# Optimization experiments

Hardware: AMD Instinct MI355X
Metric: run time of the kernel (lower is better)

Reference implementation:

```python
import jax, jax.numpy as jnp
import numpy as np

B, H, W, C = 32, 128, 128, 128
WS, SS, NH = 2, 1, 8          # window_size, shift_size, num_heads
SZ = WS * WS                   # tokens per window (4)
HD = C // NH                   # head dim
NW = (H // WS) * (W // WS)     # windows per image


def _rel_pos_index():
    coords = np.stack(np.meshgrid(np.arange(WS), np.arange(WS), indexing='ij')).reshape(2, -1)
    rel = (coords[:, :, None] - coords[:, None, :]).transpose(1, 2, 0)
    rel[:, :, 0] += WS - 1
    rel[:, :, 1] += WS - 1
    rel[:, :, 0] *= 2 * WS - 1
    return rel.sum(-1).reshape(-1)  # [SZ*SZ]


def _attn_mask():
    # shifted-window mask, computed once on host (static constant)
    img = np.zeros((H, W))
    cnt = 0
    sl = (slice(0, -WS), slice(-WS, -SS), slice(-SS, None))
    for hs in sl:
        for ws_ in sl:
            img[hs, ws_] = cnt
            cnt += 1
    mw = img.reshape(H // WS, WS, W // WS, WS).transpose(0, 2, 1, 3).reshape(-1, SZ)  # [NW, SZ]
    diff = mw[:, None, :] - mw[:, :, None]
    return np.where(diff != 0, -100.0, 0.0).astype(np.float32)  # [NW, SZ, SZ]

_RPI = _rel_pos_index()
_MASK = _attn_mask()


def setup_inputs() -> dict:
    key = jax.random.key(0)
    ks = jax.random.split(key, 6)
    return {
        'x': jax.random.normal(ks[0], (B, H * W, C), jnp.float32),
        'qkv_w': jax.random.normal(ks[1], (C, 3 * C), jnp.float32) * 0.02,
        'qkv_b': jnp.zeros((3 * C,), jnp.float32),
        'proj_w': jax.random.normal(ks[2], (C, C), jnp.float32) * 0.02,
        'proj_b': jnp.zeros((C,), jnp.float32),
        'rpb_table': jax.random.normal(ks[3], (9, NH), jnp.float32) * 0.02,
        'gamma1': jnp.ones((C,), jnp.float32),
        'beta1': jnp.zeros((C,), jnp.float32),
        'gamma2': jnp.ones((C,), jnp.float32),
        'beta2': jnp.zeros((C,), jnp.float32),
        'mlp_w1': jax.random.normal(ks[4], (C, 256), jnp.float32) * 0.02,
        'mlp_b1': jnp.zeros((256,), jnp.float32),
        'mlp_w2': jax.random.normal(ks[5], (256, C), jnp.float32) * 0.02,
        'mlp_b2': jnp.zeros((C,), jnp.float32),
    }


def _ln(z, g, b):
    m = z.mean(-1, keepdims=True)
    v = ((z - m) ** 2).mean(-1, keepdims=True)
    return (z - m) * jax.lax.rsqrt(v + 1e-5) * g + b


def reference(x, qkv_w, qkv_b, proj_w, proj_b, rpb_table,
              gamma1, beta1, gamma2, beta2, mlp_w1, mlp_b1, mlp_w2, mlp_b2):
    mask = jnp.asarray(_MASK)                      # [NW, SZ, SZ]
    skip = x
    h = _ln(x, gamma1, beta1).reshape(B, H, W, C)
    h = jnp.roll(h, (-SS, -SS), axis=(1, 2))       # cyclic shift
    # window partition -> [B*NW, SZ, C]
    hw = h.reshape(B, H // WS, WS, W // WS, WS, C).transpose(0, 1, 3, 2, 4, 5).reshape(B * NW, SZ, C)
    qkv = (hw @ qkv_w + qkv_b).reshape(B * NW, SZ, 3, NH, HD).transpose(2, 0, 3, 1, 4)
    q, k, v = qkv[0] * (HD ** -0.5), qkv[1], qkv[2]
    attn = jnp.einsum('nhid,nhjd->nhij', q, k)     # [B*NW, NH, SZ, SZ]
    rpb = rpb_table[_RPI].reshape(SZ, SZ, NH).transpose(2, 0, 1)
    attn = attn + rpb[None]
    attn = attn.reshape(B, NW, NH, SZ, SZ) + mask[None, :, None]
    attn = jax.nn.softmax(attn, axis=-1).reshape(B * NW, NH, SZ, SZ)
    o = jnp.einsum('nhij,nhjd->nhid', attn, v).transpose(0, 2, 1, 3).reshape(B * NW, SZ, C)
    o = o @ proj_w + proj_b
    # window reverse -> [B, H, W, C]
    o = o.reshape(B, H // WS, W // WS, WS, WS, C).transpose(0, 1, 3, 2, 4, 5).reshape(B, H, W, C)
    o = jnp.roll(o, (SS, SS), axis=(1, 2)).reshape(B, H * W, C)
    h = skip + o
    skip2 = h
    m = _ln(h, gamma2, beta2)
    m = jax.nn.gelu(m @ mlp_w1 + mlp_b1, approximate=False) @ mlp_w2 + mlp_b2
    return skip2 + m
```

## Files before the change

kernel.cpp:

```cpp
#include <hip/hip_runtime.h>
#include <math.h>


typedef __attribute__((ext_vector_type(8))) short short8;
typedef __attribute__((ext_vector_type(8))) unsigned short ushort8;
typedef __attribute__((ext_vector_type(4))) unsigned short ushort4v;
typedef __attribute__((ext_vector_type(4))) float f32x4;

#define MFMA __builtin_amdgcn_mfma_f32_16x16x32_bf16

__device__ inline unsigned short f2bf(float f) {
  union { float f; unsigned u; } v; v.f = f;
  unsigned r = (v.u + 0x7fffu + ((v.u >> 16) & 1u)) >> 16;
  return (unsigned short)r;
}
__device__ inline float bf2f(unsigned short s) {
  union { unsigned u; float f; } v; v.u = ((unsigned)s) << 16;
  return v.f;
}
__device__ inline void ld16(const unsigned short* p, float* o) {
  ushort8 a = *(const ushort8*)p;
  ushort8 b = *(const ushort8*)(p + 8);
  #pragma unroll
  for (int t = 0; t < 8; ++t) { o[t] = bf2f(a[t]); o[8 + t] = bf2f(b[t]); }
}

namespace {

__global__ __launch_bounds__(256) void prep_weights(
    const float* __restrict__ qkv_w, const float* __restrict__ proj_w,
    const float* __restrict__ w1, const float* __restrict__ w2,
    unsigned short* __restrict__ ws)
{
  const int idx = blockIdx.x * 256 + threadIdx.x;
  float v;
  if (idx < 49152) {
    const int n = idx >> 7, k = idx & 127; v = qkv_w[k * 384 + n];
  } else if (idx < 65536) {
    const int l = idx - 49152; const int n = l >> 7, k = l & 127;
    v = proj_w[k * 128 + n];
  } else if (idx < 98304) {
    const int l = idx - 65536; const int n = l >> 7, k = l & 127;
    v = w1[k * 256 + n];
  } else {
    const int l = idx - 98304; const int n = l >> 8, k = l & 255;
    v = w2[k * 128 + n];
  }
  ws[idx] = f2bf(v);
}

__global__ __launch_bounds__(256, 3) void swin_fused(
    const float* __restrict__ x,
    const unsigned short* __restrict__ wsw,
    const float* __restrict__ qkv_b,
    const float* __restrict__ proj_b,
    const float* __restrict__ rpb,
    const float* __restrict__ g1,
    const float* __restrict__ b1,
    const float* __restrict__ g2,
    const float* __restrict__ bt2,
    const float* __restrict__ bias1,
    const float* __restrict__ bias2,
    float* __restrict__ out)
{
  __shared__ __align__(16) unsigned char smem[52480];
  int* gsrc = (int*)smem;
  unsigned short (*Asm)[136]  = (unsigned short(*)[136])(smem + 256);
  unsigned short (*qkvh)[200] = (unsigned short(*)[200])(smem + 17664);
  unsigned short (*ohsc)[72]  = (unsigned short(*)[72])(smem + 43264);
  unsigned short (*ys)[136]   = (unsigned short(*)[136])(smem + 256);
  unsigned short (*hid0)[72]  = (unsigned short(*)[72])(smem + 17664);
  unsigned short (*hid1)[72]  = (unsigned short(*)[72])(smem + 26880);

  const int tid = threadIdx.x;
  const int n0 = blockIdx.x * 16;

  {
    const int r = tid >> 2;
    const int part = tid & 3;
    const int n = n0 + (r >> 2);
    const int s = r & 3;
    const int b = n >> 12;
    const int rem = n & 4095;
    const int wh = rem >> 6, wwi = rem & 63;
    const int hp = (2 * wh + (s >> 1) + 1) & 127;
    const int wp = (2 * wwi + (s & 1) + 1) & 127;
    const int src = (b << 14) + (hp << 7) + wp;
    if (part == 0) gsrc[r] = src;
    const float4* xr = (const float4*)(x + (size_t)src * 128 + part * 32);
    float4 v[8];
    float sum = 0.f, ssq = 0.f;
    #pragma unroll
    for (int i = 0; i < 8; ++i) {
      v[i] = xr[i];
      sum += v[i].x + v[i].y + v[i].z + v[i].w;
      ssq += v[i].x * v[i].x + v[i].y * v[i].y + v[i].z * v[i].z + v[i].w * v[i].w;
    }
    sum += __shfl_xor(sum, 1, 4); sum += __shfl_xor(sum, 2, 4);
    ssq += __shfl_xor(ssq, 1, 4); ssq += __shfl_xor(ssq, 2, 4);
    const float mean = sum * 0.0078125f;
    const float var = ssq * 0.0078125f - mean * mean;
    const float rstd = rsqrtf(var + 1e-5f);
    const int c0 = part * 32;
    #pragma unroll
    for (int i = 0; i < 8; ++i) {
      const int c = c0 + i * 4;
      const float4 gv = *(const float4*)(g1 + c);
      const float4 bv = *(const float4*)(b1 + c);
      ushort4v h4;
      h4.x = f2bf((v[i].x - mean) * rstd * gv.x + bv.x);
      h4.y = f2bf((v[i].y - mean) * rstd * gv.y + bv.y);
      h4.z = f2bf((v[i].z - mean) * rstd * gv.z + bv.z);
      h4.w = f2bf((v[i].w - mean) * rstd * gv.w + bv.w);
      *(ushort4v*)&Asm[r][c] = h4;
    }
  }
  __syncthreads();

  const int lane = tid & 63;
  const int wave = tid >> 6;
  const int l15 = lane & 15;
  const int quad = lane >> 4;

  const unsigned short* qkv_wt = wsw;
  const unsigned short* proj_wt = wsw + 49152;

  f32x4 accp[4][2] = {};

  for (int g = 0; g < 2; ++g) {
    {
      f32x4 acc[4][3] = {};
      const int nq = g * 64 + wave * 16 + l15;
      const unsigned short* bq = qkv_wt + (size_t)nq * 128;
      const unsigned short* bk = qkv_wt + (size_t)(128 + nq) * 128;
      const unsigned short* bv = qkv_wt + (size_t)(256 + nq) * 128;
      #pragma unroll
      for (int ks = 0; ks < 4; ++ks) {
        const int k0 = ks * 32 + quad * 8;
        const short8 fq = *(const short8*)(bq + k0);
        const short8 fk = *(const short8*)(bk + k0);
        const short8 fv = *(const short8*)(bv + k0);
        #pragma unroll
        for (int rf = 0; rf < 4; ++rf) {
          const short8 af = *(const short8*)&Asm[rf * 16 + l15][k0];
          acc[rf][0] = MFMA(af, fq, acc[rf][0], 0, 0, 0);
          acc[rf][1] = MFMA(af, fk, acc[rf][1], 0, 0, 0);
          acc[rf][2] = MFMA(af, fv, acc[rf][2], 0, 0, 0);
        }
      }
      const float bbq = qkv_b[nq];
      const float bbk = qkv_b[128 + nq];
      const float bbv = qkv_b[256 + nq];
      #pragma unroll
      for (int rf = 0; rf < 4; ++rf) {
        #pragma unroll
        for (int r = 0; r < 4; ++r) {
          const int row = rf * 16 + quad * 4 + r;
          qkvh[row][wave * 16 + l15]       = f2bf((acc[rf][0][r] + bbq) * 0.25f);
          qkvh[row][64 + wave * 16 + l15]  = f2bf(acc[rf][1][r] + bbk);
          qkvh[row][128 + wave * 16 + l15] = f2bf(acc[rf][2][r] + bbv);
        }
      }
    }
    __syncthreads();

    {
      const int w = tid >> 4;
      const int hl = (tid >> 2) & 3;
      const int i = tid & 3;
      const int h = g * 4 + hl;
      const int row_i = 4 * w + i;
      const int n = n0 + w;
      const int rem = n & 4095;
      const int wh = rem >> 6, wwi = rem & 63;
      const int yi = 2 * wh + (i >> 1);
      const int xi = 2 * wwi + (i & 1);
      const int regi = ((yi < 126) ? 0 : ((yi == 126) ? 1 : 2)) * 3
                     + ((xi < 126) ? 0 : ((xi == 126) ? 1 : 2));
      float q[16];
      ld16(&qkvh[row_i][hl * 16], q);
      float p[4];
      #pragma unroll
      for (int j = 0; j < 4; ++j) {
        float kk[16];
        ld16(&qkvh[4 * w + j][64 + hl * 16], kk);
        float d = 0.f;
        #pragma unroll
        for (int dd = 0; dd < 16; ++dd) d += q[dd] * kk[dd];
        const int idx = ((i >> 1) - (j >> 1) + 1) * 3 + ((i & 1) - (j & 1) + 1);
        d += rpb[idx * 8 + h];
        const int yj = 2 * wh + (j >> 1);
        const int xj = 2 * wwi + (j & 1);
        const int regj = ((yj < 126) ? 0 : ((yj == 126) ? 1 : 2)) * 3
                       + ((xj < 126) ? 0 : ((xj == 126) ? 1 : 2));
        if (regi != regj) d -= 100.f;
        p[j] = d;
      }
      const float mx = fmaxf(fmaxf(p[0], p[1]), fmaxf(p[2], p[3]));
      float es = 0.f;
      #pragma unroll
      for (int j = 0; j < 4; ++j) { p[j] = expf(p[j] - mx); es += p[j]; }
      const float inv = 1.f / es;
      float o[16];
      #pragma unroll
      for (int dd = 0; dd < 16; ++dd) o[dd] = 0.f;
      #pragma unroll
      for (int j = 0; j < 4; ++j) {
        float vv[16];
        ld16(&qkvh[4 * w + j][128 + hl * 16], vv);
        #pragma unroll
        for (int dd = 0; dd < 16; ++dd) o[dd] += p[j] * vv[dd];
      }
      ushort8 oa, ob;
      #pragma unroll
      for (int dd = 0; dd < 8; ++dd) {
        oa[dd] = f2bf(o[dd] * inv);
        ob[dd] = f2bf(o[8 + dd] * inv);
      }
      *(ushort8*)&ohsc[row_i][hl * 16] = oa;
      *(ushort8*)&ohsc[row_i][hl * 16 + 8] = ob;
    }
    __syncthreads();

    {
      #pragma unroll
      for (int ks = 0; ks < 2; ++ks) {
        const int k0 = ks * 32 + quad * 8;
        const short8 f0 = *(const short8*)(proj_wt + (size_t)(wave * 32 + l15) * 128 + g * 64 + k0);
        const short8 f1 = *(const short8*)(proj_wt + (size_t)(wave * 32 + 16 + l15) * 128 + g * 64 + k0);
        #pragma unroll
        for (int rf = 0; rf < 4; ++rf) {
          const short8 af = *(const short8*)&ohsc[rf * 16 + l15][k0];
          accp[rf][0] = MFMA(af, f0, accp[rf][0], 0, 0, 0);
          accp[rf][1] = MFMA(af, f1, accp[rf][1], 0, 0, 0);
        }
      }
    }
  }

  #pragma unroll
  for (int rf = 0; rf < 4; ++rf) {
    #pragma unroll
    for (int r = 0; r < 4; ++r) {
      const int row = rf * 16 + quad * 4 + r;
      const int src = gsrc[row];
      float* orow = out + (size_t)src * 128;
      const float* xr = x + (size_t)src * 128;
      #pragma unroll
      for (int nt = 0; nt < 2; ++nt) {
        const int col = wave * 32 + nt * 16 + l15;
        orow[col] = accp[rf][nt][r] + proj_b[col] + xr[col];
      }
    }
  }
  __syncthreads();

  {
    const int r = tid >> 2;
    const int part = tid & 3;
    const int src = gsrc[r];
    const float4* yr = (const float4*)(out + (size_t)src * 128 + part * 32);
    float4 v[8];
    float sum = 0.f, ssq = 0.f;
    #pragma unroll
    for (int i = 0; i < 8; ++i) {
      v[i] = yr[i];
      sum += v[i].x + v[i].y + v[i].z + v[i].w;
      ssq += v[i].x * v[i].x + v[i].y * v[i].y + v[i].z * v[i].z + v[i].w * v[i].w;
    }
    sum += __shfl_xor(sum, 1, 4); sum += __shfl_xor(sum, 2, 4);
    ssq += __shfl_xor(ssq, 1, 4); ssq += __shfl_xor(ssq, 2, 4);
    const float mean = sum * 0.0078125f;
    const float var = ssq * 0.0078125f - mean * mean;
    const float rstd = rsqrtf(var + 1e-5f);
    const int c0 = part * 32;
    #pragma unroll
    for (int i = 0; i < 8; ++i) {
      const int c = c0 + i * 4;
      const float4 gv = *(const float4*)(g2 + c);
      const float4 bv = *(const float4*)(bt2 + c);
      ushort4v h4;
      h4.x = f2bf((v[i].x - mean) * rstd * gv.x + bv.x);
      h4.y = f2bf((v[i].y - mean) * rstd * gv.y + bv.y);
      h4.z = f2bf((v[i].z - mean) * rstd * gv.z + bv.z);
      h4.w = f2bf((v[i].w - mean) * rstd * gv.w + bv.w);
      *(ushort4v*)&ys[r][c] = h4;
    }
  }
  __syncthreads();

  const unsigned short* w1t = wsw + 65536;
  const unsigned short* w2t = wsw + 98304;
  f32x4 am[4][2] = {};

  auto G1 = [&](int c, unsigned short (*hb)[72]) {
    f32x4 hacc[4] = {};
    const int ht = c * 4 + wave;
    const unsigned short* arow = w1t + (size_t)(ht * 16 + l15) * 128;
    #pragma unroll
    for (int ks = 0; ks < 4; ++ks) {
      const int k0 = ks * 32 + quad * 8;
      const short8 af = *(const short8*)(arow + k0);
      #pragma unroll
      for (int mt = 0; mt < 4; ++mt) {
        const short8 bf = *(const short8*)&ys[mt * 16 + l15][k0];
        hacc[mt] = MFMA(af, bf, hacc[mt], 0, 0, 0);
      }
    }
    const int hbase = ht * 16 + quad * 4;
    const float4 bb = *(const float4*)(bias1 + hbase);
    #pragma unroll
    for (int mt = 0; mt < 4; ++mt) {
      ushort4v pk;
      #pragma unroll
      for (int r = 0; r < 4; ++r) {
        float v = hacc[mt][r] + ((const float*)&bb)[r];
        v = 0.5f * v * (1.f + erff(v * 0.70710678118654752f));
        pk[r] = f2bf(v);
      }
      *(ushort4v*)&hb[mt * 16 + l15][wave * 16 + quad * 4] = pk;
    }
  };
  auto G2 = [&](int c, const unsigned short (*hb)[72]) {
    #pragma unroll
    for (int ks = 0; ks < 2; ++ks) {
      const int k0 = ks * 32 + quad * 8;
      const int kg = c * 64 + k0;
      const short8 f0 = *(const short8*)(w2t + (size_t)(wave * 32 + l15) * 256 + kg);
      const short8 f1 = *(const short8*)(w2t + (size_t)(wave * 32 + 16 + l15) * 256 + kg);
      #pragma unroll
      for (int rf = 0; rf < 4; ++rf) {
        const short8 af = *(const short8*)&hb[rf * 16 + l15][k0];
        am[rf][0] = MFMA(af, f0, am[rf][0], 0, 0, 0);
        am[rf][1] = MFMA(af, f1, am[rf][1], 0, 0, 0);
      }
    }
  };

  G1(0, hid0);
  __syncthreads();
  G1(1, hid1); G2(0, hid0);
  __syncthreads();
  G1(2, hid0); G2(1, hid1);
  __syncthreads();
  G1(3, hid1); G2(2, hid0);
  __syncthreads();
  G2(3, hid1);

  #pragma unroll
  for (int rf = 0; rf < 4; ++rf) {
    #pragma unroll
    for (int r = 0; r < 4; ++r) {
      const int row = rf * 16 + quad * 4 + r;
      const int src = gsrc[row];
      float* orow = out + (size_t)src * 128;
      #pragma unroll
      for (int nt = 0; nt < 2; ++nt) {
        const int col = wave * 32 + nt * 16 + l15;
        orow[col] += bias2[col] + am[rf][nt][r];
      }
    }
  }
}

}

extern "C" void kernel_launch(void* const* d_in, const int* in_sizes, int n_in,
                              void* d_out, int out_size, void* d_ws, size_t ws_size,
                              hipStream_t stream) {
  const float* x      = (const float*)d_in[0];
  const float* qkv_w  = (const float*)d_in[1];
  const float* qkv_b  = (const float*)d_in[2];
  const float* proj_w = (const float*)d_in[3];
  const float* proj_b = (const float*)d_in[4];
  const float* rpb    = (const float*)d_in[5];
  const float* g1     = (const float*)d_in[6];
  const float* b1     = (const float*)d_in[7];
  const float* g2     = (const float*)d_in[8];
  const float* b2     = (const float*)d_in[9];
  const float* w1     = (const float*)d_in[10];
  const float* bias1  = (const float*)d_in[11];
  const float* w2     = (const float*)d_in[12];
  const float* bias2  = (const float*)d_in[13];
  float* out = (float*)d_out;
  unsigned short* wsw = (unsigned short*)d_ws;

  hipLaunchKernelGGL(prep_weights, dim3(512), dim3(256), 0, stream,
                     qkv_w, proj_w, w1, w2, wsw);
  hipLaunchKernelGGL(swin_fused, dim3(8192), dim3(256), 0, stream,
                     x, wsw, qkv_b, proj_b, rpb, g1, b1, g2, b2, bias1, bias2, out);
}
```

Measured before the change: 895.9 us.

## Run window attention on MFMA, keep residual in registers, shrink LDS

The scalar per-thread QK and PV dot products become 16x16x32 MFMAs, with operands staged through small per-wave LDS tiles and ds_bpermute shuffles. Each wave now handles one head per group, and qkv and proj weights are preloaded into registers ahead of use. The intermediate residual is no longer written to global memory and re-read for the second LayerNorm; it stays in accumulators, with LN2 statistics reduced through shuffles and a small LDS buffer. LDS drops enough to raise the occupancy hint from 3 to 4 blocks. The cost is higher register pressure from the preloaded weights, plus zero-padded MFMAs that waste part of each instruction.

```diff
diff --git a/kernel.cpp b/kernel.cpp
--- a/kernel.cpp
+++ b/kernel.cpp
@@ -14,16 +14,10 @@
   unsigned r = (v.u + 0x7fffu + ((v.u >> 16) & 1u)) >> 16;
   return (unsigned short)r;
 }
-__device__ inline float bf2f(unsigned short s) {
-  union { unsigned u; float f; } v; v.u = ((unsigned)s) << 16;
-  return v.f;
-}
-__device__ inline void ld16(const unsigned short* p, float* o) {
-  ushort8 a = *(const ushort8*)p;
-  ushort8 b = *(const ushort8*)(p + 8);
-  #pragma unroll
-  for (int t = 0; t < 8; ++t) { o[t] = bf2f(a[t]); o[8 + t] = bf2f(b[t]); }
-}
+__device__ inline unsigned pk2(float a, float b) {
+  return (unsigned)f2bf(a) | ((unsigned)f2bf(b) << 16);
+}
+union V4 { unsigned u[4]; short8 s; };
 
 namespace {
 
@@ -49,7 +43,7 @@
   ws[idx] = f2bf(v);
 }
 
-__global__ __launch_bounds__(256, 3) void swin_fused(
+__global__ __launch_bounds__(256, 4) void swin_fused(
     const float* __restrict__ x,
     const unsigned short* __restrict__ wsw,
     const float* __restrict__ qkv_b,
@@ -63,21 +57,47 @@
     const float* __restrict__ bias2,
     float* __restrict__ out)
 {
-  __shared__ __align__(16) unsigned char smem[52480];
+  __shared__ __align__(16) unsigned char smem[40192];
   int* gsrc = (int*)smem;
-  unsigned short (*Asm)[136]  = (unsigned short(*)[136])(smem + 256);
-  unsigned short (*qkvh)[200] = (unsigned short(*)[200])(smem + 17664);
-  unsigned short (*ohsc)[72]  = (unsigned short(*)[72])(smem + 43264);
-  unsigned short (*ys)[136]   = (unsigned short(*)[136])(smem + 256);
-  unsigned short (*hid0)[72]  = (unsigned short(*)[72])(smem + 17664);
-  unsigned short (*hid1)[72]  = (unsigned short(*)[72])(smem + 26880);
+  unsigned short (*Asm)[136] = (unsigned short(*)[136])(smem + 256);
+  unsigned short (*ys)[136]  = (unsigned short(*)[136])(smem + 256);
+  unsigned short (*ohs)[136] = (unsigned short(*)[136])(smem + 22784);
+  unsigned short (*hid0)[72] = (unsigned short(*)[72])(smem + 17664);
+  unsigned short (*hid1)[72] = (unsigned short(*)[72])(smem + 26880);
+  float* part = (float*)(smem + 17664);
 
   const int tid = threadIdx.x;
   const int n0 = blockIdx.x * 16;
+  const int lane = tid & 63;
+  const int wave = tid >> 6;
+  const int l15 = lane & 15;
+  const int quad = lane >> 4;
+  const f32x4 fz = {0.f, 0.f, 0.f, 0.f};
+
+  const unsigned short* qkv_wt = wsw;
+  const unsigned short* proj_wt = wsw + 49152;
+
+  unsigned short (*sq)[20] = (unsigned short(*)[20])(smem + 17664 + wave * 1280);
+  unsigned short (*sk)[20] = (unsigned short(*)[20])(smem + 17664 + wave * 1280 + 640);
+
+  short8 w0q[4], w0k[4], w0v[4];
+  {
+    const int nq = wave * 16 + l15;
+    const unsigned short* bq = qkv_wt + (size_t)nq * 128;
+    const unsigned short* bk = qkv_wt + (size_t)(128 + nq) * 128;
+    const unsigned short* bv = qkv_wt + (size_t)(256 + nq) * 128;
+    #pragma unroll
+    for (int ks = 0; ks < 4; ++ks) {
+      const int k0 = ks * 32 + quad * 8;
+      w0q[ks] = *(const short8*)(bq + k0);
+      w0k[ks] = *(const short8*)(bk + k0);
+      w0v[ks] = *(const short8*)(bv + k0);
+    }
+  }
 
   {
     const int r = tid >> 2;
-    const int part = tid & 3;
+    const int partc = tid & 3;
     const int n = n0 + (r >> 2);
     const int s = r & 3;
     const int b = n >> 12;
@@ -86,8 +106,8 @@
     const int hp = (2 * wh + (s >> 1) + 1) & 127;
     const int wp = (2 * wwi + (s & 1) + 1) & 127;
     const int src = (b << 14) + (hp << 7) + wp;
-    if (part == 0) gsrc[r] = src;
-    const float4* xr = (const float4*)(x + (size_t)src * 128 + part * 32);
+    if (partc == 0) gsrc[r] = src;
+    const float4* xr = (const float4*)(x + (size_t)src * 128 + partc * 32);
     float4 v[8];
     float sum = 0.f, ssq = 0.f;
     #pragma unroll
@@ -101,7 +121,7 @@
     const float mean = sum * 0.0078125f;
     const float var = ssq * 0.0078125f - mean * mean;
     const float rstd = rsqrtf(var + 1e-5f);
-    const int c0 = part * 32;
+    const int c0 = partc * 32;
     #pragma unroll
     for (int i = 0; i < 8; ++i) {
       const int c = c0 + i * 4;
@@ -117,77 +137,56 @@
   }
   __syncthreads();
 
-  const int lane = tid & 63;
-  const int wave = tid >> 6;
-  const int l15 = lane & 15;
-  const int quad = lane >> 4;
-
-  const unsigned short* qkv_wt = wsw;
-  const unsigned short* proj_wt = wsw + 49152;
-
-  f32x4 accp[4][2] = {};
-
-  for (int g = 0; g < 2; ++g) {
-    {
-      f32x4 acc[4][3] = {};
-      const int nq = g * 64 + wave * 16 + l15;
-      const unsigned short* bq = qkv_wt + (size_t)nq * 128;
-      const unsigned short* bk = qkv_wt + (size_t)(128 + nq) * 128;
-      const unsigned short* bv = qkv_wt + (size_t)(256 + nq) * 128;
-      #pragma unroll
-      for (int ks = 0; ks < 4; ++ks) {
-        const int k0 = ks * 32 + quad * 8;
-        const short8 fq = *(const short8*)(bq + k0);
-        const short8 fk = *(const short8*)(bk + k0);
-        const short8 fv = *(const short8*)(bv + k0);
-        #pragma unroll
-        for (int rf = 0; rf < 4; ++rf) {
-          const short8 af = *(const short8*)&Asm[rf * 16 + l15][k0];
-          acc[rf][0] = MFMA(af, fq, acc[rf][0], 0, 0, 0);
-          acc[rf][1] = MFMA(af, fk, acc[rf][1], 0, 0, 0);
-          acc[rf][2] = MFMA(af, fv, acc[rf][2], 0, 0, 0);
-        }
-      }
-      const float bbq = qkv_b[nq];
-      const float bbk = qkv_b[128 + nq];
-      const float bbv = qkv_b[256 + nq];
+  auto QKV = [&](const short8* wq, const short8* wk, const short8* wv,
+                 f32x4 (&acc)[4][3]) {
+    #pragma unroll
+    for (int ks = 0; ks < 4; ++ks) {
+      const int k0 = ks * 32 + quad * 8;
       #pragma unroll
       for (int rf = 0; rf < 4; ++rf) {
-        #pragma unroll
-        for (int r = 0; r < 4; ++r) {
-          const int row = rf * 16 + quad * 4 + r;
-          qkvh[row][wave * 16 + l15]       = f2bf((acc[rf][0][r] + bbq) * 0.25f);
-          qkvh[row][64 + wave * 16 + l15]  = f2bf(acc[rf][1][r] + bbk);
-          qkvh[row][128 + wave * 16 + l15] = f2bf(acc[rf][2][r] + bbv);
-        }
-      }
-    }
-    __syncthreads();
-
-    {
-      const int w = tid >> 4;
-      const int hl = (tid >> 2) & 3;
-      const int i = tid & 3;
-      const int h = g * 4 + hl;
-      const int row_i = 4 * w + i;
-      const int n = n0 + w;
+        const short8 af = *(const short8*)&Asm[rf * 16 + l15][k0];
+        acc[rf][0] = MFMA(af, wq[ks], acc[rf][0], 0, 0, 0);
+        acc[rf][1] = MFMA(af, wk[ks], acc[rf][1], 0, 0, 0);
+        acc[rf][2] = MFMA(af, wv[ks], acc[rf][2], 0, 0, 0);
+      }
+    }
+  };
+
+  auto ATTN = [&](int g, f32x4 (&acc)[4][3]) {
+    const int h = g * 4 + wave;
+    const int nq = g * 64 + wave * 16 + l15;
+    const float bbq = qkv_b[nq];
+    const float bbk = qkv_b[128 + nq];
+    const float bbv = qkv_b[256 + nq];
+    #pragma unroll
+    for (int wg = 0; wg < 4; ++wg) {
+      #pragma unroll
+      for (int r = 0; r < 4; ++r) {
+        sq[quad * 4 + r][l15] = f2bf((acc[wg][0][r] + bbq) * 0.25f);
+        sk[quad * 4 + r][l15] = f2bf(acc[wg][1][r] + bbk);
+      }
+      const unsigned pv0 = pk2(acc[wg][2][0] + bbv, acc[wg][2][1] + bbv);
+      const unsigned pv1 = pk2(acc[wg][2][2] + bbv, acc[wg][2][3] + bbv);
+      short8 ka = {}, qb = {};
+      if (quad < 2) {
+        ka = *(const short8*)&sk[l15][quad * 8];
+        qb = *(const short8*)&sq[l15][quad * 8];
+      }
+      const f32x4 s = MFMA(ka, qb, fz, 0, 0, 0);
+      const int i2 = l15 & 3;
+      const int wl = wg * 4 + (l15 >> 2);
+      const int n = n0 + wl;
       const int rem = n & 4095;
       const int wh = rem >> 6, wwi = rem & 63;
-      const int yi = 2 * wh + (i >> 1);
-      const int xi = 2 * wwi + (i & 1);
+      const int yi = 2 * wh + (i2 >> 1);
+      const int xi = 2 * wwi + (i2 & 1);
       const int regi = ((yi < 126) ? 0 : ((yi == 126) ? 1 : 2)) * 3
                      + ((xi < 126) ? 0 : ((xi == 126) ? 1 : 2));
-      float q[16];
-      ld16(&qkvh[row_i][hl * 16], q);
       float p[4];
       #pragma unroll
       for (int j = 0; j < 4; ++j) {
-        float kk[16];
-        ld16(&qkvh[4 * w + j][64 + hl * 16], kk);
-        float d = 0.f;
-        #pragma unroll
-        for (int dd = 0; dd < 16; ++dd) d += q[dd] * kk[dd];
-        const int idx = ((i >> 1) - (j >> 1) + 1) * 3 + ((i & 1) - (j & 1) + 1);
+        float d = s[j];
+        const int idx = ((i2 >> 1) - (j >> 1) + 1) * 3 + ((i2 & 1) - (j & 1) + 1);
         d += rpb[idx * 8 + h];
         const int yj = 2 * wh + (j >> 1);
         const int xj = 2 * wwi + (j & 1);
@@ -199,41 +198,93 @@
       const float mx = fmaxf(fmaxf(p[0], p[1]), fmaxf(p[2], p[3]));
       float es = 0.f;
       #pragma unroll
-      for (int j = 0; j < 4; ++j) { p[j] = expf(p[j] - mx); es += p[j]; }
+      for (int j = 0; j < 4; ++j) {
+        p[j] = exp2f((p[j] - mx) * 1.44269504f);
+        es += p[j];
+      }
       const float inv = 1.f / es;
-      float o[16];
-      #pragma unroll
-      for (int dd = 0; dd < 16; ++dd) o[dd] = 0.f;
-      #pragma unroll
-      for (int j = 0; j < 4; ++j) {
-        float vv[16];
-        ld16(&qkvh[4 * w + j][128 + hl * 16], vv);
-        #pragma unroll
-        for (int dd = 0; dd < 16; ++dd) o[dd] += p[j] * vv[dd];
-      }
-      ushort8 oa, ob;
-      #pragma unroll
-      for (int dd = 0; dd < 8; ++dd) {
-        oa[dd] = f2bf(o[dd] * inv);
-        ob[dd] = f2bf(o[8 + dd] * inv);
-      }
-      *(ushort8*)&ohsc[row_i][hl * 16] = oa;
-      *(ushort8*)&ohsc[row_i][hl * 16 + 8] = ob;
-    }
-    __syncthreads();
-
-    {
-      #pragma unroll
-      for (int ks = 0; ks < 2; ++ks) {
-        const int k0 = ks * 32 + quad * 8;
-        const short8 f0 = *(const short8*)(proj_wt + (size_t)(wave * 32 + l15) * 128 + g * 64 + k0);
-        const short8 f1 = *(const short8*)(proj_wt + (size_t)(wave * 32 + 16 + l15) * 128 + g * 64 + k0);
-        #pragma unroll
-        for (int rf = 0; rf < 4; ++rf) {
-          const short8 af = *(const short8*)&ohsc[rf * 16 + l15][k0];
-          accp[rf][0] = MFMA(af, f0, accp[rf][0], 0, 0, 0);
-          accp[rf][1] = MFMA(af, f1, accp[rf][1], 0, 0, 0);
-        }
+      const unsigned pd0 = pk2(p[0] * inv, p[1] * inv);
+      const unsigned pd1 = pk2(p[2] * inv, p[3] * inv);
+      const int srcp = (((l15 >> 2) << 4) | l15) << 2;
+      const unsigned a0 = (unsigned)__builtin_amdgcn_ds_bpermute(srcp, (int)pd0);
+      const unsigned a1 = (unsigned)__builtin_amdgcn_ds_bpermute(srcp, (int)pd1);
+      const bool take = (quad == (l15 >> 3));
+      const bool lo = ((l15 >> 2) & 1) == 0;
+      V4 pa;
+      pa.u[0] = (take && lo)  ? a0 : 0u;
+      pa.u[1] = (take && lo)  ? a1 : 0u;
+      pa.u[2] = (take && !lo) ? a0 : 0u;
+      pa.u[3] = (take && !lo) ? a1 : 0u;
+      const int qs = (quad < 2) ? (quad * 2) : 0;
+      const int sva = (qs * 16 + l15) << 2;
+      const int svb = ((qs + 1) * 16 + l15) << 2;
+      V4 vb;
+      vb.u[0] = (unsigned)__builtin_amdgcn_ds_bpermute(sva, (int)pv0);
+      vb.u[1] = (unsigned)__builtin_amdgcn_ds_bpermute(sva, (int)pv1);
+      vb.u[2] = (unsigned)__builtin_amdgcn_ds_bpermute(svb, (int)pv0);
+      vb.u[3] = (unsigned)__builtin_amdgcn_ds_bpermute(svb, (int)pv1);
+      if (quad >= 2) { vb.u[0] = 0u; vb.u[1] = 0u; vb.u[2] = 0u; vb.u[3] = 0u; }
+      const f32x4 o = MFMA(pa.s, vb.s, fz, 0, 0, 0);
+      #pragma unroll
+      for (int r = 0; r < 4; ++r)
+        ohs[wg * 16 + quad * 4 + r][h * 16 + l15] = f2bf(o[r]);
+    }
+  };
+
+  f32x4 acc0[4][3] = {};
+  QKV(w0q, w0k, w0v, acc0);
+  short8 w1q[4], w1k[4], w1v[4];
+  {
+    const int nq = 64 + wave * 16 + l15;
+    const unsigned short* bq = qkv_wt + (size_t)nq * 128;
+    const unsigned short* bk = qkv_wt + (size_t)(128 + nq) * 128;
+    const unsigned short* bv = qkv_wt + (size_t)(256 + nq) * 128;
+    #pragma unroll
+    for (int ks = 0; ks < 4; ++ks) {
+      const int k0 = ks * 32 + quad * 8;
+      w1q[ks] = *(const short8*)(bq + k0);
+      w1k[ks] = *(const short8*)(bk + k0);
+      w1v[ks] = *(const short8*)(bv + k0);
+    }
+  }
+  ATTN(0, acc0);
+
+  f32x4 acc1[4][3] = {};
+  QKV(w1q, w1k, w1v, acc1);
+  short8 pw[2][4];
+  #pragma unroll
+  for (int nt = 0; nt < 2; ++nt) {
+    const unsigned short* br = proj_wt + (size_t)(wave * 32 + nt * 16 + l15) * 128;
+    #pragma unroll
+    for (int ks = 0; ks < 4; ++ks)
+      pw[nt][ks] = *(const short8*)(br + ks * 32 + quad * 8);
+  }
+  ATTN(1, acc1);
+  __syncthreads();
+
+  f32x4 accp[4][2] = {};
+  #pragma unroll
+  for (int ks = 0; ks < 4; ++ks) {
+    const int k0 = ks * 32 + quad * 8;
+    #pragma unroll
+    for (int rf = 0; rf < 4; ++rf) {
+      const short8 af = *(const short8*)&ohs[rf * 16 + l15][k0];
+      accp[rf][0] = MFMA(af, pw[0][ks], accp[rf][0], 0, 0, 0);
+      accp[rf][1] = MFMA(af, pw[1][ks], accp[rf][1], 0, 0, 0);
+    }
+  }
+  const int ca = wave * 32 + l15;
+  const int cb = wave * 32 + 16 + l15;
+  {
+    const float pba = proj_b[ca], pbb = proj_b[cb];
+    #pragma unroll
+    for (int rf = 0; rf < 4; ++rf) {
+      #pragma unroll
+      for (int r = 0; r < 4; ++r) {
+        const int src = gsrc[rf * 16 + quad * 4 + r];
+        const float* xr = x + (size_t)src * 128;
+        accp[rf][0][r] += pba + xr[ca];
+        accp[rf][1][r] += pbb + xr[cb];
       }
     }
   }
@@ -242,49 +293,38 @@
   for (int rf = 0; rf < 4; ++rf) {
     #pragma unroll
     for (int r = 0; r < 4; ++r) {
-      const int row = rf * 16 + quad * 4 + r;
-      const int src = gsrc[row];
-      float* orow = out + (size_t)src * 128;
-      const float* xr = x + (size_t)src * 128;
-      #pragma unroll
-      for (int nt = 0; nt < 2; ++nt) {
-        const int col = wave * 32 + nt * 16 + l15;
-        orow[col] = accp[rf][nt][r] + proj_b[col] + xr[col];
-      }
-    }
-  }
-  __syncthreads();
-
-  {
-    const int r = tid >> 2;
-    const int part = tid & 3;
-    const int src = gsrc[r];
-    const float4* yr = (const float4*)(out + (size_t)src * 128 + part * 32);
-    float4 v[8];
-    float sum = 0.f, ssq = 0.f;
-    #pragma unroll
-    for (int i = 0; i < 8; ++i) {
-      v[i] = yr[i];
-      sum += v[i].x + v[i].y + v[i].z + v[i].w;
-      ssq += v[i].x * v[i].x + v[i].y * v[i].y + v[i].z * v[i].z + v[i].w * v[i].w;
-    }
-    sum += __shfl_xor(sum, 1, 4); sum += __shfl_xor(sum, 2, 4);
-    ssq += __shfl_xor(ssq, 1, 4); ssq += __shfl_xor(ssq, 2, 4);
-    const float mean = sum * 0.0078125f;
-    const float var = ssq * 0.0078125f - mean * mean;
-    const float rstd = rsqrtf(var + 1e-5f);
-    const int c0 = part * 32;
-    #pragma unroll
-    for (int i = 0; i < 8; ++i) {
-      const int c = c0 + i * 4;
-      const float4 gv = *(const float4*)(g2 + c);
-      const float4 bv = *(const float4*)(bt2 + c);
-      ushort4v h4;
-      h4.x = f2bf((v[i].x - mean) * rstd * gv.x + bv.x);
-      h4.y = f2bf((v[i].y - mean) * rstd * gv.y + bv.y);
-      h4.z = f2bf((v[i].z - mean) * rstd * gv.z + bv.z);
-      h4.w = f2bf((v[i].w - mean) * rstd * gv.w + bv.w);
-      *(ushort4v*)&ys[r][c] = h4;
+      float sv = accp[rf][0][r] + accp[rf][1][r];
+      float qv = accp[rf][0][r] * accp[rf][0][r] + accp[rf][1][r] * accp[rf][1][r];
+      sv += __shfl_xor(sv, 1, 16); sv += __shfl_xor(sv, 2, 16);
+      sv += __shfl_xor(sv, 4, 16); sv += __shfl_xor(sv, 8, 16);
+      qv += __shfl_xor(qv, 1, 16); qv += __shfl_xor(qv, 2, 16);
+      qv += __shfl_xor(qv, 4, 16); qv += __shfl_xor(qv, 8, 16);
+      if (l15 == 0) {
+        float2 pq; pq.x = sv; pq.y = qv;
+        *(float2*)&part[(rf * 16 + quad * 4 + r) * 8 + wave * 2] = pq;
+      }
+    }
+  }
+  __syncthreads();
+
+  {
+    const float g2a = g2[ca], g2b = g2[cb];
+    const float bta = bt2[ca], btb = bt2[cb];
+    #pragma unroll
+    for (int rf = 0; rf < 4; ++rf) {
+      #pragma unroll
+      for (int r = 0; r < 4; ++r) {
+        const int row = rf * 16 + quad * 4 + r;
+        const float2 p0 = *(const float2*)&part[row * 8 + 0];
+        const float2 p1 = *(const float2*)&part[row * 8 + 2];
+        const float2 p2 = *(const float2*)&part[row * 8 + 4];
+        const float2 p3 = *(const float2*)&part[row * 8 + 6];
+        const float mean = (p0.x + p1.x + p2.x + p3.x) * 0.0078125f;
+        const float ex2 = (p0.y + p1.y + p2.y + p3.y) * 0.0078125f;
+        const float rstd = rsqrtf(ex2 - mean * mean + 1e-5f);
+        ys[row][ca] = f2bf((accp[rf][0][r] - mean) * rstd * g2a + bta);
+        ys[row][cb] = f2bf((accp[rf][1][r] - mean) * rstd * g2b + btb);
+      }
     }
   }
   __syncthreads();
@@ -326,8 +366,8 @@
     for (int ks = 0; ks < 2; ++ks) {
       const int k0 = ks * 32 + quad * 8;
       const int kg = c * 64 + k0;
-      const short8 f0 = *(const short8*)(w2t + (size_t)(wave * 32 + l15) * 256 + kg);
-      const short8 f1 = *(const short8*)(w2t + (size_t)(wave * 32 + 16 + l15) * 256 + kg);
+      const short8 f0 = *(const short8*)(w2t + (size_t)ca * 256 + kg);
+      const short8 f1 = *(const short8*)(w2t + (size_t)cb * 256 + kg);
       #pragma unroll
       for (int rf = 0; rf < 4; ++rf) {
         const short8 af = *(const short8*)&hb[rf * 16 + l15][k0];
@@ -347,17 +387,16 @@
   __syncthreads();
   G2(3, hid1);
 
-  #pragma unroll
-  for (int rf = 0; rf < 4; ++rf) {
-    #pragma unroll
-    for (int r = 0; r < 4; ++r) {
-      const int row = rf * 16 + quad * 4 + r;
-      const int src = gsrc[row];
-      float* orow = out + (size_t)src * 128;
-      #pragma unroll
-      for (int nt = 0; nt < 2; ++nt) {
-        const int col = wave * 32 + nt * 16 + l15;
-        orow[col] += bias2[col] + am[rf][nt][r];
+  {
+    const float b2a = bias2[ca], b2b = bias2[cb];
+    #pragma unroll
+    for (int rf = 0; rf < 4; ++rf) {
+      #pragma unroll
+      for (int r = 0; r < 4; ++r) {
+        const int src = gsrc[rf * 16 + quad * 4 + r];
+        float* orow = out + (size_t)src * 128;
+        orow[ca] = accp[rf][0][r] + b2a + am[rf][0][r];
+        orow[cb] = accp[rf][1][r] + b2b + am[rf][1][r];
       }
     }
   }
```

Result: no change. 892.1 us (-0.4%).
